# Kernel tuning notes

Hardware: AMD Instinct MI355X
Metric: run time of the kernel (lower is better)

## Reference

```python
import jax, jax.numpy as jnp
import numpy as np

N, E, D, H = 50000, 800000, 64, 8
DH = D // H
EPS = 1e-5


def _bn(x, gamma, beta):
    # BatchNorm1d in training mode: biased variance over the node axis
    m = x.mean(axis=0)
    v = ((x - m) ** 2).mean(axis=0)
    return (x - m) * jax.lax.rsqrt(v + EPS) * gamma + beta


def setup_inputs() -> dict:
    key = jax.random.key(0)
    ks = jax.random.split(key, 12)
    s_in = 1.0 / np.sqrt(D)
    s_ff = 1.0 / np.sqrt(2 * D)
    inp = {
        "h": jax.random.normal(ks[0], (N, D), dtype=jnp.float32),
        "src": jax.random.randint(ks[1], (E,), 0, N, dtype=jnp.int32),
        "dst": jax.random.randint(ks[2], (E,), 0, N, dtype=jnp.int32),
        "Wq": jax.random.normal(ks[3], (D, D), dtype=jnp.float32) * s_in,
        "bq": jnp.zeros((D,), jnp.float32),
        "Wk": jax.random.normal(ks[4], (D, D), dtype=jnp.float32) * s_in,
        "bk": jnp.zeros((D,), jnp.float32),
        "Wv": jax.random.normal(ks[5], (D, D), dtype=jnp.float32) * s_in,
        "bv": jnp.zeros((D,), jnp.float32),
        "g1": jnp.ones((D,), jnp.float32),
        "b1": jnp.zeros((D,), jnp.float32),
        "W1": jax.random.normal(ks[6], (D, 2 * D), dtype=jnp.float32) * s_in,
        "bb1": jnp.zeros((2 * D,), jnp.float32),
        "W2": jax.random.normal(ks[7], (2 * D, D), dtype=jnp.float32) * s_ff,
        "bb2": jnp.zeros((D,), jnp.float32),
        "g2": jnp.ones((D,), jnp.float32),
        "b2": jnp.zeros((D,), jnp.float32),
    }
    return inp


def reference(h, src, dst, Wq, bq, Wk, bk, Wv, bv, g1, b1, W1, bb1, W2, bb2, g2, b2):
    scale = np.sqrt(DH).astype(np.float32)
    Q = (h @ Wq + bq).reshape(N, H, DH)
    K = (h @ Wk + bk).reshape(N, H, DH)
    V = (h @ Wv + bv).reshape(N, H, DH)

    # per-edge score: K[src] . Q[dst], clamped/scaled exp  -> [E, H]
    score = jnp.sum(K[src] * Q[dst], axis=-1)
    score = jnp.exp(jnp.clip(score / scale, -5.0, 5.0))

    # weighted-value and normalizer scatter-sums onto dst nodes
    wV = jax.ops.segment_sum(V[src] * score[:, :, None], dst, num_segments=N)  # [N,H,DH]
    z = jax.ops.segment_sum(score, dst, num_segments=N)  # [N,H]

    safe_z = jnp.where(z == 0, 1.0, z)
    head = jnp.where((z == 0)[:, :, None], 0.0, wV / safe_z[:, :, None])  # nan -> 0
    attn = head.reshape(N, D)

    h1 = _bn(h + attn, g1, b1)
    ffn = jax.nn.relu(h1 @ W1 + bb1) @ W2 + bb2
    out = _bn(h1 + ffn, g2, b2)
    return out
```

## Files before the change

kernel.cpp:

```cpp
#include <hip/hip_runtime.h>
#include <hip/hip_fp16.h>
#include <math.h>

#define N_NODES 50000
#define E_EDGES 800000
#define EPS_BN  1e-5f
#define INV_N   (1.0f / N_NODES)
#define SCAN_BLOCKS 196
#define QKV_BLOCKS  782
#define HIST_BLOCKS 3125

__global__ __launch_bounds__(256) void qkv_hist_kernel(
    const float* __restrict__ h,
    const float* __restrict__ Wq, const float* __restrict__ bq,
    const float* __restrict__ Wk, const float* __restrict__ bk,
    const float* __restrict__ Wv, const float* __restrict__ bv,
    float* __restrict__ Q, __half* __restrict__ KV,
    const int* __restrict__ dst, int* __restrict__ count)
{
    __shared__ float  xs[64][68];
    __shared__ __half Wqh[64][64];
    __shared__ __half Wkh[64][64];
    __shared__ __half Wvh[64][64];
    const int t = threadIdx.x;

    if (blockIdx.x >= QKV_BLOCKS) {
        const int e = (blockIdx.x - QKV_BLOCKS) * 256 + t;
        if (e < E_EDGES) atomicAdd(&count[dst[e]], 1);
        return;
    }

    const int tx = t & 15;
    const int ty = t >> 4;
    const int row0 = blockIdx.x * 64;

    {
        __half2* wq = (__half2*)&Wqh[0][0];
        __half2* wk = (__half2*)&Wkh[0][0];
        __half2* wv = (__half2*)&Wvh[0][0];
        #pragma unroll
        for (int k = 0; k < 4; ++k) {
            const int i = t + k * 256;
            const float4 a = *(const float4*)(Wq + i * 4);
            wq[i * 2]     = __floats2half2_rn(a.x, a.y);
            wq[i * 2 + 1] = __floats2half2_rn(a.z, a.w);
            const float4 b = *(const float4*)(Wk + i * 4);
            wk[i * 2]     = __floats2half2_rn(b.x, b.y);
            wk[i * 2 + 1] = __floats2half2_rn(b.z, b.w);
            const float4 c = *(const float4*)(Wv + i * 4);
            wv[i * 2]     = __floats2half2_rn(c.x, c.y);
            wv[i * 2 + 1] = __floats2half2_rn(c.z, c.w);
        }
    }

    #pragma unroll
    for (int k = 0; k < 4; ++k) {
        const int i  = t + k * 256;
        const int r  = i >> 4;
        const int c4 = (i & 15) * 4;
        float4 v = make_float4(0.f, 0.f, 0.f, 0.f);
        if (row0 + r < N_NODES)
            v = *(const float4*)(h + (size_t)(row0 + r) * 64 + c4);
        *(float4*)(&xs[r][c4]) = v;
    }
    __syncthreads();

    const int c0 = tx * 4;
    float4 aq[4], ak[4], av[4];
    const float4 bq4 = *(const float4*)(bq + c0);
    const float4 bk4 = *(const float4*)(bk + c0);
    const float4 bv4 = *(const float4*)(bv + c0);
    #pragma unroll
    for (int i = 0; i < 4; ++i) { aq[i] = bq4; ak[i] = bk4; av[i] = bv4; }

    #pragma unroll 4
    for (int c = 0; c < 64; ++c) {
        const __half2* qp = (const __half2*)&Wqh[c][c0];
        const __half2* kp = (const __half2*)&Wkh[c][c0];
        const __half2* vp = (const __half2*)&Wvh[c][c0];
        const float2 wq0 = __half22float2(qp[0]);
        const float2 wq1 = __half22float2(qp[1]);
        const float2 wk0 = __half22float2(kp[0]);
        const float2 wk1 = __half22float2(kp[1]);
        const float2 wv0 = __half22float2(vp[0]);
        const float2 wv1 = __half22float2(vp[1]);
        #pragma unroll
        for (int i = 0; i < 4; ++i) {
            const float xv = xs[ty * 4 + i][c];
            aq[i].x = fmaf(xv, wq0.x, aq[i].x); aq[i].y = fmaf(xv, wq0.y, aq[i].y);
            aq[i].z = fmaf(xv, wq1.x, aq[i].z); aq[i].w = fmaf(xv, wq1.y, aq[i].w);
            ak[i].x = fmaf(xv, wk0.x, ak[i].x); ak[i].y = fmaf(xv, wk0.y, ak[i].y);
            ak[i].z = fmaf(xv, wk1.x, ak[i].z); ak[i].w = fmaf(xv, wk1.y, ak[i].w);
            av[i].x = fmaf(xv, wv0.x, av[i].x); av[i].y = fmaf(xv, wv0.y, av[i].y);
            av[i].z = fmaf(xv, wv1.x, av[i].z); av[i].w = fmaf(xv, wv1.y, av[i].w);
        }
    }
    #pragma unroll
    for (int i = 0; i < 4; ++i) {
        const int row = row0 + ty * 4 + i;
        if (row < N_NODES) {
            *(float4*)(Q + (size_t)row * 64 + c0) = aq[i];
            __half* kvp = KV + (size_t)row * 128;
            *(__half2*)(kvp + c0)          = __floats2half2_rn(ak[i].x, ak[i].y);
            *(__half2*)(kvp + c0 + 2)      = __floats2half2_rn(ak[i].z, ak[i].w);
            *(__half2*)(kvp + 64 + c0)     = __floats2half2_rn(av[i].x, av[i].y);
            *(__half2*)(kvp + 64 + c0 + 2) = __floats2half2_rn(av[i].z, av[i].w);
        }
    }
}

__global__ __launch_bounds__(256) void scanA_kernel(
    const int* __restrict__ count,
    int* __restrict__ rowStart, int* __restrict__ blockSums)
{
    __shared__ int ls[256];
    const int t = threadIdx.x;
    const int i = blockIdx.x * 256 + t;
    const int v = (i < N_NODES) ? count[i] : 0;
    ls[t] = v;
    __syncthreads();
    #pragma unroll
    for (int off = 1; off < 256; off <<= 1) {
        const int u = (t >= off) ? ls[t - off] : 0;
        __syncthreads();
        ls[t] += u;
        __syncthreads();
    }
    if (i < N_NODES) rowStart[i] = ls[t] - v;
    if (t == 255) blockSums[blockIdx.x] = ls[255];
}

__global__ __launch_bounds__(256) void scanBC_kernel(
    int* __restrict__ rowStart, int* __restrict__ cursor,
    const int* __restrict__ blockSums)
{
    __shared__ int ls[256];
    const int t = threadIdx.x;
    const int v = (t < SCAN_BLOCKS) ? blockSums[t] : 0;
    ls[t] = v;
    __syncthreads();
    #pragma unroll
    for (int off = 1; off < 256; off <<= 1) {
        const int u = (t >= off) ? ls[t - off] : 0;
        __syncthreads();
        ls[t] += u;
        __syncthreads();
    }
    const int exc = ls[t] - v;
    __syncthreads();
    ls[t] = exc;
    __syncthreads();
    const int boff = ls[blockIdx.x];
    const int i = blockIdx.x * 256 + t;
    if (i < N_NODES) {
        const int r = rowStart[i] + boff;
        rowStart[i] = r;
        cursor[i]   = r;
    }
    if (i == 0) rowStart[N_NODES] = E_EDGES;
}

__global__ __launch_bounds__(256) void scatter_kernel(
    const int* __restrict__ src, const int* __restrict__ dst,
    int* __restrict__ cursor, int* __restrict__ srcSorted)
{
    const int e0 = blockIdx.x * 512 + threadIdx.x;
    const int e1 = e0 + 256;
    const bool h0 = e0 < E_EDGES;
    const bool h1 = e1 < E_EDGES;
    const int s0 = h0 ? src[e0] : 0;
    const int d0 = h0 ? dst[e0] : 0;
    const int s1 = h1 ? src[e1] : 0;
    const int d1 = h1 ? dst[e1] : 0;
    if (h0) srcSorted[atomicAdd(&cursor[d0], 1)] = s0;
    if (h1) srcSorted[atomicAdd(&cursor[d1], 1)] = s1;
}

__global__ __launch_bounds__(256) void gather_edge_kernel(
    const float* __restrict__ h,
    const float* __restrict__ Q, const __half* __restrict__ KV,
    const int* __restrict__ rowStart, const int* __restrict__ srcSorted,
    float* __restrict__ x, float* __restrict__ s1, float* __restrict__ sq1)
{
    const int lane = threadIdx.x & 63;
    const int wave = threadIdx.x >> 6;
    const int hh = lane & 7;
    const int el = lane >> 3;
    float bsum[8], bsq[8];
    #pragma unroll
    for (int j = 0; j < 8; ++j) { bsum[j] = 0.0f; bsq[j] = 0.0f; }

    const int nodeStep = gridDim.x * 4;
    for (int n = blockIdx.x * 4 + wave; n < N_NODES; n += nodeStep) {
        const int start = rowStart[n];
        const int end   = rowStart[n + 1];
        const size_t qb = (size_t)n * 64 + hh * 8;
        const float4 q0 = *(const float4*)(Q + qb);
        const float4 q1 = *(const float4*)(Q + qb + 4);
        float a0=0,a1=0,a2=0,a3=0,a4=0,a5=0,a6=0,a7=0,zacc=0;
        for (int e = start + el; e < end; e += 16) {
            const int s0 = srcSorted[e];
            const int e1 = e + 8;
            const bool has1 = (e1 < end);
            const int s1i = has1 ? srcSorted[e1] : s0;
            const __half* kv0 = KV + (size_t)s0 * 128 + hh * 8;
            const __half* kv1 = KV + (size_t)s1i * 128 + hh * 8;
            const float4 kraw0 = *(const float4*)(kv0);
            const float4 vraw0 = *(const float4*)(kv0 + 64);
            const float4 kraw1 = *(const float4*)(kv1);
            const float4 vraw1 = *(const float4*)(kv1 + 64);

            {
                const __half2* kh = (const __half2*)&kraw0;
                const float2 ka = __half22float2(kh[0]);
                const float2 kb = __half22float2(kh[1]);
                const float2 kc = __half22float2(kh[2]);
                const float2 kd = __half22float2(kh[3]);
                float sc = ka.x*q0.x + ka.y*q0.y + kb.x*q0.z + kb.y*q0.w
                         + kc.x*q1.x + kc.y*q1.y + kd.x*q1.z + kd.y*q1.w;
                sc *= 0.35355339059327373f;
                sc = fminf(5.0f, fmaxf(-5.0f, sc));
                const float p = __expf(sc);
                const __half2* vh = (const __half2*)&vraw0;
                const float2 va = __half22float2(vh[0]);
                const float2 vb = __half22float2(vh[1]);
                const float2 vc = __half22float2(vh[2]);
                const float2 vd = __half22float2(vh[3]);
                a0 = fmaf(p, va.x, a0); a1 = fmaf(p, va.y, a1);
                a2 = fmaf(p, vb.x, a2); a3 = fmaf(p, vb.y, a3);
                a4 = fmaf(p, vc.x, a4); a5 = fmaf(p, vc.y, a5);
                a6 = fmaf(p, vd.x, a6); a7 = fmaf(p, vd.y, a7);
                zacc += p;
            }
            if (has1) {
                const __half2* kh = (const __half2*)&kraw1;
                const float2 ka = __half22float2(kh[0]);
                const float2 kb = __half22float2(kh[1]);
                const float2 kc = __half22float2(kh[2]);
                const float2 kd = __half22float2(kh[3]);
                float sc = ka.x*q0.x + ka.y*q0.y + kb.x*q0.z + kb.y*q0.w
                         + kc.x*q1.x + kc.y*q1.y + kd.x*q1.z + kd.y*q1.w;
                sc *= 0.35355339059327373f;
                sc = fminf(5.0f, fmaxf(-5.0f, sc));
                const float p = __expf(sc);
                const __half2* vh = (const __half2*)&vraw1;
                const float2 va = __half22float2(vh[0]);
                const float2 vb = __half22float2(vh[1]);
                const float2 vc = __half22float2(vh[2]);
                const float2 vd = __half22float2(vh[3]);
                a0 = fmaf(p, va.x, a0); a1 = fmaf(p, va.y, a1);
                a2 = fmaf(p, vb.x, a2); a3 = fmaf(p, vb.y, a3);
                a4 = fmaf(p, vc.x, a4); a5 = fmaf(p, vc.y, a5);
                a6 = fmaf(p, vd.x, a6); a7 = fmaf(p, vd.y, a7);
                zacc += p;
            }
        }
        #pragma unroll
        for (int m = 8; m < 64; m <<= 1) {
            a0 += __shfl_xor(a0, m, 64); a1 += __shfl_xor(a1, m, 64);
            a2 += __shfl_xor(a2, m, 64); a3 += __shfl_xor(a3, m, 64);
            a4 += __shfl_xor(a4, m, 64); a5 += __shfl_xor(a5, m, 64);
            a6 += __shfl_xor(a6, m, 64); a7 += __shfl_xor(a7, m, 64);
            zacc += __shfl_xor(zacc, m, 64);
        }
        if (el == 0) {
            const float inv = (zacc == 0.0f) ? 0.0f : 1.0f / zacc;
            const float4 h0 = *(const float4*)(h + qb);
            const float4 h1 = *(const float4*)(h + qb + 4);
            float xv[8];
            xv[0] = fmaf(a0, inv, h0.x); xv[1] = fmaf(a1, inv, h0.y);
            xv[2] = fmaf(a2, inv, h0.z); xv[3] = fmaf(a3, inv, h0.w);
            xv[4] = fmaf(a4, inv, h1.x); xv[5] = fmaf(a5, inv, h1.y);
            xv[6] = fmaf(a6, inv, h1.z); xv[7] = fmaf(a7, inv, h1.w);
            *(float4*)(x + qb)     = make_float4(xv[0], xv[1], xv[2], xv[3]);
            *(float4*)(x + qb + 4) = make_float4(xv[4], xv[5], xv[6], xv[7]);
            #pragma unroll
            for (int j = 0; j < 8; ++j) {
                bsum[j] += xv[j];
                bsq[j]  += xv[j] * xv[j];
            }
        }
    }
    __shared__ float lsm[256];
    __shared__ float lsq[256];
    if (el == 0) {
        #pragma unroll
        for (int j = 0; j < 8; ++j) {
            lsm[wave * 64 + hh * 8 + j] = bsum[j];
            lsq[wave * 64 + hh * 8 + j] = bsq[j];
        }
    }
    __syncthreads();
    if (threadIdx.x < 64) {
        const int tt = threadIdx.x;
        const float s = lsm[tt] + lsm[tt + 64] + lsm[tt + 128] + lsm[tt + 192];
        const float q = lsq[tt] + lsq[tt + 64] + lsq[tt + 128] + lsq[tt + 192];
        atomicAdd(s1 + tt, s);
        atomicAdd(sq1 + tt, q);
    }
}

__global__ __launch_bounds__(512, 4) void ffn_kernel(
    const float* __restrict__ x,
    const float* __restrict__ s1, const float* __restrict__ sq1,
    const float* __restrict__ g1, const float* __restrict__ b1,
    const float* __restrict__ W1, const float* __restrict__ bb1,
    const float* __restrict__ W2, const float* __restrict__ bb2,
    float* __restrict__ y, float* __restrict__ s2, float* __restrict__ sq2)
{
    __shared__ __half W1h[64][128];
    __shared__ __half W2h[128][64];
    __shared__ float  xs[64][64];
    __shared__ __half ts[64][128];

    const int t  = threadIdx.x;
    const int tx = t & 15;
    const int ty = t >> 4;
    const int row0 = blockIdx.x * 64;

    {
        __half2* w1p = (__half2*)&W1h[0][0];
        __half2* w2p = (__half2*)&W2h[0][0];
        #pragma unroll
        for (int k = 0; k < 4; ++k) {
            const int i = t + k * 512;
            const float4 w1 = *(const float4*)(W1 + i * 4);
            w1p[i * 2]     = __floats2half2_rn(w1.x, w1.y);
            w1p[i * 2 + 1] = __floats2half2_rn(w1.z, w1.w);
            const float4 w2 = *(const float4*)(W2 + i * 4);
            w2p[i * 2]     = __floats2half2_rn(w2.x, w2.y);
            w2p[i * 2 + 1] = __floats2half2_rn(w2.z, w2.w);
        }
    }

    {
        const int c4 = tx * 4;
        const float4 ssum = *(const float4*)(s1 + c4);
        const float4 sqs  = *(const float4*)(sq1 + c4);
        const float4 gg   = *(const float4*)(g1 + c4);
        const float4 bb   = *(const float4*)(b1 + c4);
        float4 mm, rr, A, C;
        mm.x = ssum.x * INV_N; mm.y = ssum.y * INV_N;
        mm.z = ssum.z * INV_N; mm.w = ssum.w * INV_N;
        rr.x = rsqrtf(sqs.x * INV_N - mm.x * mm.x + EPS_BN);
        rr.y = rsqrtf(sqs.y * INV_N - mm.y * mm.y + EPS_BN);
        rr.z = rsqrtf(sqs.z * INV_N - mm.z * mm.z + EPS_BN);
        rr.w = rsqrtf(sqs.w * INV_N - mm.w * mm.w + EPS_BN);
        A.x = rr.x * gg.x; C.x = bb.x - mm.x * A.x;
        A.y = rr.y * gg.y; C.y = bb.y - mm.y * A.y;
        A.z = rr.z * gg.z; C.z = bb.z - mm.z * A.z;
        A.w = rr.w * gg.w; C.w = bb.w - mm.w * A.w;
        #pragma unroll
        for (int k = 0; k < 2; ++k) {
            const int i = t + k * 512;
            const int r = i >> 4;
            float4 v = make_float4(0.f, 0.f, 0.f, 0.f);
            if (row0 + r < N_NODES) {
                const float4 xv = *(const float4*)(x + (size_t)(row0 + r) * 64 + c4);
                v.x = fmaf(xv.x, A.x, C.x);
                v.y = fmaf(xv.y, A.y, C.y);
                v.z = fmaf(xv.z, A.z, C.z);
                v.w = fmaf(xv.w, A.w, C.w);
            }
            *(float4*)(&xs[r][c4]) = v;
        }
    }
    __syncthreads();

    const int r0 = ty * 2, r1 = r0 + 1;

    {
        const int cA = tx * 4, cB = 64 + tx * 4;
        float4 aA0 = make_float4(0,0,0,0), aA1 = aA0, aB0 = aA0, aB1 = aA0;
        #pragma unroll 4
        for (int c = 0; c < 64; ++c) {
            const __half2* wAp = (const __half2*)&W1h[c][cA];
            const __half2* wBp = (const __half2*)&W1h[c][cB];
            const float2 wa0 = __half22float2(wAp[0]);
            const float2 wa1 = __half22float2(wAp[1]);
            const float2 wb0 = __half22float2(wBp[0]);
            const float2 wb1 = __half22float2(wBp[1]);
            const float x0 = xs[r0][c];
            const float x1 = xs[r1][c];
            aA0.x = fmaf(x0, wa0.x, aA0.x); aA0.y = fmaf(x0, wa0.y, aA0.y);
            aA0.z = fmaf(x0, wa1.x, aA0.z); aA0.w = fmaf(x0, wa1.y, aA0.w);
            aA1.x = fmaf(x1, wa0.x, aA1.x); aA1.y = fmaf(x1, wa0.y, aA1.y);
            aA1.z = fmaf(x1, wa1.x, aA1.z); aA1.w = fmaf(x1, wa1.y, aA1.w);
            aB0.x = fmaf(x0, wb0.x, aB0.x); aB0.y = fmaf(x0, wb0.y, aB0.y);
            aB0.z = fmaf(x0, wb1.x, aB0.z); aB0.w = fmaf(x0, wb1.y, aB0.w);
            aB1.x = fmaf(x1, wb0.x, aB1.x); aB1.y = fmaf(x1, wb0.y, aB1.y);
            aB1.z = fmaf(x1, wb1.x, aB1.z); aB1.w = fmaf(x1, wb1.y, aB1.w);
        }
        const float4 b1A = *(const float4*)(bb1 + cA);
        const float4 b1B = *(const float4*)(bb1 + cB);
        aA0.x = fmaxf(aA0.x + b1A.x, 0.f); aA0.y = fmaxf(aA0.y + b1A.y, 0.f);
        aA0.z = fmaxf(aA0.z + b1A.z, 0.f); aA0.w = fmaxf(aA0.w + b1A.w, 0.f);
        aA1.x = fmaxf(aA1.x + b1A.x, 0.f); aA1.y = fmaxf(aA1.y + b1A.y, 0.f);
        aA1.z = fmaxf(aA1.z + b1A.z, 0.f); aA1.w = fmaxf(aA1.w + b1A.w, 0.f);
        aB0.x = fmaxf(aB0.x + b1B.x, 0.f); aB0.y = fmaxf(aB0.y + b1B.y, 0.f);
        aB0.z = fmaxf(aB0.z + b1B.z, 0.f); aB0.w = fmaxf(aB0.w + b1B.w, 0.f);
        aB1.x = fmaxf(aB1.x + b1B.x, 0.f); aB1.y = fmaxf(aB1.y + b1B.y, 0.f);
        aB1.z = fmaxf(aB1.z + b1B.z, 0.f); aB1.w = fmaxf(aB1.w + b1B.w, 0.f);
        *(__half2*)&ts[r0][cA]     = __floats2half2_rn(aA0.x, aA0.y);
        *(__half2*)&ts[r0][cA + 2] = __floats2half2_rn(aA0.z, aA0.w);
        *(__half2*)&ts[r1][cA]     = __floats2half2_rn(aA1.x, aA1.y);
        *(__half2*)&ts[r1][cA + 2] = __floats2half2_rn(aA1.z, aA1.w);
        *(__half2*)&ts[r0][cB]     = __floats2half2_rn(aB0.x, aB0.y);
        *(__half2*)&ts[r0][cB + 2] = __floats2half2_rn(aB0.z, aB0.w);
        *(__half2*)&ts[r1][cB]     = __floats2half2_rn(aB1.x, aB1.y);
        *(__half2*)&ts[r1][cB + 2] = __floats2half2_rn(aB1.z, aB1.w);
    }
    __syncthreads();

    float4 s = make_float4(0,0,0,0), q = s;
    {
        const int c4 = tx * 4;
        float4 y0 = make_float4(0,0,0,0), y1 = y0;
        #pragma unroll 4
        for (int k = 0; k < 128; ++k) {
            const __half2* wp = (const __half2*)&W2h[k][c4];
            const float2 wa = __half22float2(wp[0]);
            const float2 wb = __half22float2(wp[1]);
            const float T0 = __half2float(ts[r0][k]);
            const float T1 = __half2float(ts[r1][k]);
            y0.x = fmaf(T0, wa.x, y0.x); y0.y = fmaf(T0, wa.y, y0.y);
            y0.z = fmaf(T0, wb.x, y0.z); y0.w = fmaf(T0, wb.y, y0.w);
            y1.x = fmaf(T1, wa.x, y1.x); y1.y = fmaf(T1, wa.y, y1.y);
            y1.z = fmaf(T1, wb.x, y1.z); y1.w = fmaf(T1, wb.y, y1.w);
        }
        const float4 bb = *(const float4*)(bb2 + c4);
        const float4 h0 = *(const float4*)(&xs[r0][c4]);
        const float4 h1v = *(const float4*)(&xs[r1][c4]);
        y0.x += bb.x + h0.x;  y0.y += bb.y + h0.y;
        y0.z += bb.z + h0.z;  y0.w += bb.w + h0.w;
        y1.x += bb.x + h1v.x; y1.y += bb.y + h1v.y;
        y1.z += bb.z + h1v.z; y1.w += bb.w + h1v.w;

        const bool v0 = (row0 + r0) < N_NODES;
        const bool v1 = (row0 + r1) < N_NODES;
        if (v0) *(float4*)(y + (size_t)(row0 + r0) * 64 + c4) = y0;
        if (v1) *(float4*)(y + (size_t)(row0 + r1) * 64 + c4) = y1;

        if (v0) {
            s.x += y0.x; s.y += y0.y; s.z += y0.z; s.w += y0.w;
            q.x += y0.x*y0.x; q.y += y0.y*y0.y; q.z += y0.z*y0.z; q.w += y0.w*y0.w;
        }
        if (v1) {
            s.x += y1.x; s.y += y1.y; s.z += y1.z; s.w += y1.w;
            q.x += y1.x*y1.x; q.y += y1.y*y1.y; q.z += y1.z*y1.z; q.w += y1.w*y1.w;
        }
    }
    {
        float* red = (float*)&W1h[0][0];
        const int c4 = tx * 4;
        *(float4*)(red + ty * 64 + c4)        = s;
        *(float4*)(red + (32 + ty) * 64 + c4) = q;
    }
    __syncthreads();
    if (t < 64) {
        const float* red = (const float*)&W1h[0][0];
        float ss = 0.f, qq = 0.f;
        #pragma unroll
        for (int k = 0; k < 32; ++k) {
            ss += red[k * 64 + t];
            qq += red[(32 + k) * 64 + t];
        }
        atomicAdd(s2 + t, ss);
        atomicAdd(sq2 + t, qq);
    }
}

__global__ __launch_bounds__(256) void bn2_apply_kernel(
    float* __restrict__ y,
    const float* __restrict__ s2, const float* __restrict__ sq2,
    const float* __restrict__ g2, const float* __restrict__ b2)
{
    const int c4 = (threadIdx.x & 15) * 4;
    const float4 ssum = *(const float4*)(s2 + c4);
    const float4 sqs  = *(const float4*)(sq2 + c4);
    const float4 gg   = *(const float4*)(g2 + c4);
    const float4 bb   = *(const float4*)(b2 + c4);
    float4 mm, rr, A, C;
    mm.x = ssum.x * INV_N; mm.y = ssum.y * INV_N;
    mm.z = ssum.z * INV_N; mm.w = ssum.w * INV_N;
    rr.x = rsqrtf(sqs.x * INV_N - mm.x * mm.x + EPS_BN);
    rr.y = rsqrtf(sqs.y * INV_N - mm.y * mm.y + EPS_BN);
    rr.z = rsqrtf(sqs.z * INV_N - mm.z * mm.z + EPS_BN);
    rr.w = rsqrtf(sqs.w * INV_N - mm.w * mm.w + EPS_BN);
    A.x = rr.x * gg.x; C.x = bb.x - mm.x * A.x;
    A.y = rr.y * gg.y; C.y = bb.y - mm.y * A.y;
    A.z = rr.z * gg.z; C.z = bb.z - mm.z * A.z;
    A.w = rr.w * gg.w; C.w = bb.w - mm.w * A.w;

    const int total4 = N_NODES * 16;
    const int stride = gridDim.x * blockDim.x;
    for (int i = blockIdx.x * blockDim.x + threadIdx.x; i < total4; i += stride) {
        float4 v = *((float4*)y + i);
        v.x = fmaf(v.x, A.x, C.x);
        v.y = fmaf(v.y, A.y, C.y);
        v.z = fmaf(v.z, A.z, C.z);
        v.w = fmaf(v.w, A.w, C.w);
        *((float4*)y + i) = v;
    }
}

extern "C" void kernel_launch(void* const* d_in, const int* in_sizes, int n_in,
                              void* d_out, int out_size, void* d_ws, size_t ws_size,
                              hipStream_t stream)
{
    const float* h   = (const float*)d_in[0];
    const int*   src = (const int*)d_in[1];
    const int*   dst = (const int*)d_in[2];
    const float* Wq  = (const float*)d_in[3];
    const float* bq  = (const float*)d_in[4];
    const float* Wk  = (const float*)d_in[5];
    const float* bk  = (const float*)d_in[6];
    const float* Wv  = (const float*)d_in[7];
    const float* bv  = (const float*)d_in[8];
    const float* g1  = (const float*)d_in[9];
    const float* b1  = (const float*)d_in[10];
    const float* W1  = (const float*)d_in[11];
    const float* bb1 = (const float*)d_in[12];
    const float* W2  = (const float*)d_in[13];
    const float* bb2 = (const float*)d_in[14];
    const float* g2  = (const float*)d_in[15];
    const float* b2  = (const float*)d_in[16];
    float* out = (float*)d_out;

    float* ws = (float*)d_ws;
    const size_t ND = (size_t)N_NODES * 64;
    float* Q  = ws;
    __half* KV = (__half*)(ws + ND);
    float* x  = Q;
    int* srcSorted = (int*)(ws + 3 * ND);
    int* count     = srcSorted + E_EDGES;
    float* st      = (float*)(count + N_NODES);
    int* rowStart  = (int*)(st + 512);
    int* cursor    = rowStart + N_NODES + 1;
    int* blockSums = cursor + N_NODES;
    float* s1 = st,       *sq1 = st + 64;
    float* s2 = st + 256, *sq2 = st + 320;

    hipMemsetAsync(count, 0, (N_NODES + 512) * sizeof(int), stream);

    qkv_hist_kernel<<<QKV_BLOCKS + HIST_BLOCKS, 256, 0, stream>>>(
        h, Wq, bq, Wk, bk, Wv, bv, Q, KV, dst, count);
    scanA_kernel<<<SCAN_BLOCKS, 256, 0, stream>>>(count, rowStart, blockSums);
    scanBC_kernel<<<SCAN_BLOCKS, 256, 0, stream>>>(rowStart, cursor, blockSums);
    scatter_kernel<<<(E_EDGES + 511) / 512, 256, 0, stream>>>(
        src, dst, cursor, srcSorted);
    gather_edge_kernel<<<1024, 256, 0, stream>>>(h, Q, KV, rowStart, srcSorted,
                                                 x, s1, sq1);
    ffn_kernel<<<(N_NODES + 63) / 64, 512, 0, stream>>>(
        x, s1, sq1, g1, b1, W1, bb1, W2, bb2, out, s2, sq2);
    bn2_apply_kernel<<<2048, 256, 0, stream>>>(out, s2, sq2, g2, b2);
}
```

Measured before the change: 304.0 us.

## Store KV head-major and assign one head per block in edge gather

KV is now stored head-major as [head][node][16 halves], holding each head's K and V slice contiguously. Each block of the gather kernel handles a single head, and each group of 8 lanes handles one node's edges for that head. Work is split across 8 blocks per node chunk, so a block's random gathers touch only one head's 1/8-sized KV region, which should improve L2 hit rate. The cost is that Q, rowStart and srcSorted are read 8 times, and each lane group has less edge parallelism per node.

After: 298.4 us. About the same (-1.8%).

```diff
diff --git a/kernel.cpp b/kernel.cpp
--- a/kernel.cpp
+++ b/kernel.cpp
@@ -100,11 +100,11 @@
         const int row = row0 + ty * 4 + i;
         if (row < N_NODES) {
             *(float4*)(Q + (size_t)row * 64 + c0) = aq[i];
-            __half* kvp = KV + (size_t)row * 128;
-            *(__half2*)(kvp + c0)          = __floats2half2_rn(ak[i].x, ak[i].y);
-            *(__half2*)(kvp + c0 + 2)      = __floats2half2_rn(ak[i].z, ak[i].w);
-            *(__half2*)(kvp + 64 + c0)     = __floats2half2_rn(av[i].x, av[i].y);
-            *(__half2*)(kvp + 64 + c0 + 2) = __floats2half2_rn(av[i].z, av[i].w);
+            __half* kvp = KV + ((size_t)(c0 >> 3) * N_NODES + row) * 16 + (c0 & 7);
+            *(__half2*)(kvp)         = __floats2half2_rn(ak[i].x, ak[i].y);
+            *(__half2*)(kvp + 2)     = __floats2half2_rn(ak[i].z, ak[i].w);
+            *(__half2*)(kvp + 8)     = __floats2half2_rn(av[i].x, av[i].y);
+            *(__half2*)(kvp + 8 + 2) = __floats2half2_rn(av[i].z, av[i].w);
         }
     }
 }
@@ -184,31 +184,40 @@
 {
     const int lane = threadIdx.x & 63;
     const int wave = threadIdx.x >> 6;
-    const int hh = lane & 7;
-    const int el = lane >> 3;
+    const int slot = lane & 7;
+    const int ns   = lane >> 3;
+    const int hh   = blockIdx.x & 7;
+    const int chunk0  = blockIdx.x >> 3;
+    const int nChunks = gridDim.x >> 3;
+    const __half* __restrict__ KVh = KV + (size_t)hh * N_NODES * 16;
+
     float bsum[8], bsq[8];
     #pragma unroll
     for (int j = 0; j < 8; ++j) { bsum[j] = 0.0f; bsq[j] = 0.0f; }
 
-    const int nodeStep = gridDim.x * 4;
-    for (int n = blockIdx.x * 4 + wave; n < N_NODES; n += nodeStep) {
-        const int start = rowStart[n];
-        const int end   = rowStart[n + 1];
-        const size_t qb = (size_t)n * 64 + hh * 8;
-        const float4 q0 = *(const float4*)(Q + qb);
-        const float4 q1 = *(const float4*)(Q + qb + 4);
+    for (int chunk = chunk0; chunk * 32 < N_NODES; chunk += nChunks) {
+        const int n = chunk * 32 + wave * 8 + ns;
+        const bool valid = (n < N_NODES);
+        int start = 0, end = 0;
+        float4 q0 = make_float4(0.f, 0.f, 0.f, 0.f), q1 = q0;
+        if (valid) {
+            start = rowStart[n];
+            end   = rowStart[n + 1];
+            q0 = *(const float4*)(Q + (size_t)n * 64 + hh * 8);
+            q1 = *(const float4*)(Q + (size_t)n * 64 + hh * 8 + 4);
+        }
         float a0=0,a1=0,a2=0,a3=0,a4=0,a5=0,a6=0,a7=0,zacc=0;
-        for (int e = start + el; e < end; e += 16) {
+        for (int e = start + slot; e < end; e += 16) {
             const int s0 = srcSorted[e];
             const int e1 = e + 8;
             const bool has1 = (e1 < end);
             const int s1i = has1 ? srcSorted[e1] : s0;
-            const __half* kv0 = KV + (size_t)s0 * 128 + hh * 8;
-            const __half* kv1 = KV + (size_t)s1i * 128 + hh * 8;
+            const __half* kv0 = KVh + (size_t)s0 * 16;
+            const __half* kv1 = KVh + (size_t)s1i * 16;
             const float4 kraw0 = *(const float4*)(kv0);
-            const float4 vraw0 = *(const float4*)(kv0 + 64);
+            const float4 vraw0 = *(const float4*)(kv0 + 8);
             const float4 kraw1 = *(const float4*)(kv1);
-            const float4 vraw1 = *(const float4*)(kv1 + 64);
+            const float4 vraw1 = *(const float4*)(kv1 + 8);
 
             {
                 const __half2* kh = (const __half2*)&kraw0;
@@ -256,24 +265,26 @@
             }
         }
         #pragma unroll
-        for (int m = 8; m < 64; m <<= 1) {
+        for (int m = 1; m < 8; m <<= 1) {
             a0 += __shfl_xor(a0, m, 64); a1 += __shfl_xor(a1, m, 64);
             a2 += __shfl_xor(a2, m, 64); a3 += __shfl_xor(a3, m, 64);
             a4 += __shfl_xor(a4, m, 64); a5 += __shfl_xor(a5, m, 64);
             a6 += __shfl_xor(a6, m, 64); a7 += __shfl_xor(a7, m, 64);
             zacc += __shfl_xor(zacc, m, 64);
         }
-        if (el == 0) {
+        if (slot == 0 && valid) {
             const float inv = (zacc == 0.0f) ? 0.0f : 1.0f / zacc;
-            const float4 h0 = *(const float4*)(h + qb);
-            const float4 h1 = *(const float4*)(h + qb + 4);
+            const float4 h0 = *(const float4*)(h + (size_t)n * 64 + hh * 8);
+            const float4 h1 = *(const float4*)(h + (size_t)n * 64 + hh * 8 + 4);
             float xv[8];
             xv[0] = fmaf(a0, inv, h0.x); xv[1] = fmaf(a1, inv, h0.y);
             xv[2] = fmaf(a2, inv, h0.z); xv[3] = fmaf(a3, inv, h0.w);
             xv[4] = fmaf(a4, inv, h1.x); xv[5] = fmaf(a5, inv, h1.y);
             xv[6] = fmaf(a6, inv, h1.z); xv[7] = fmaf(a7, inv, h1.w);
-            *(float4*)(x + qb)     = make_float4(xv[0], xv[1], xv[2], xv[3]);
-            *(float4*)(x + qb + 4) = make_float4(xv[4], xv[5], xv[6], xv[7]);
+            *(float4*)(x + (size_t)n * 64 + hh * 8)     =
+                make_float4(xv[0], xv[1], xv[2], xv[3]);
+            *(float4*)(x + (size_t)n * 64 + hh * 8 + 4) =
+                make_float4(xv[4], xv[5], xv[6], xv[7]);
             #pragma unroll
             for (int j = 0; j < 8; ++j) {
                 bsum[j] += xv[j];
@@ -281,22 +292,23 @@
             }
         }
     }
-    __shared__ float lsm[256];
-    __shared__ float lsq[256];
-    if (el == 0) {
+    __shared__ float lsm[32][8];
+    __shared__ float lsq[32][8];
+    if (slot == 0) {
         #pragma unroll
         for (int j = 0; j < 8; ++j) {
-            lsm[wave * 64 + hh * 8 + j] = bsum[j];
-            lsq[wave * 64 + hh * 8 + j] = bsq[j];
-        }
-    }
-    __syncthreads();
-    if (threadIdx.x < 64) {
+            lsm[wave * 8 + ns][j] = bsum[j];
+            lsq[wave * 8 + ns][j] = bsq[j];
+        }
+    }
+    __syncthreads();
+    if (threadIdx.x < 8) {
         const int tt = threadIdx.x;
-        const float s = lsm[tt] + lsm[tt + 64] + lsm[tt + 128] + lsm[tt + 192];
-        const float q = lsq[tt] + lsq[tt + 64] + lsq[tt + 128] + lsq[tt + 192];
-        atomicAdd(s1 + tt, s);
-        atomicAdd(sq1 + tt, q);
+        float ss = 0.f, qq = 0.f;
+        #pragma unroll
+        for (int k = 0; k < 32; ++k) { ss += lsm[k][tt]; qq += lsq[k][tt]; }
+        atomicAdd(s1 + hh * 8 + tt, ss);
+        atomicAdd(sq1 + hh * 8 + tt, qq);
     }
 }
 
```
